# Kernel tuning notes

Hardware: AMD Instinct MI355X
Metric: run time of the kernel (lower is better)

Reference implementation:

```python
import jax, jax.numpy as jnp
import numpy as np

INPUT_SIZE = 64
HIDDEN_SIZE = 512
OUTPUT_SIZE = 1
BATCH = 128
SEQ = 1024


def setup_inputs() -> dict:
    key = jax.random.key(0)
    ks = jax.random.split(key, 7)
    H, I, O = HIDDEN_SIZE, INPUT_SIZE, OUTPUT_SIZE
    s = 1.0 / np.sqrt(H)  # PyTorch LSTM init scale
    x = jax.random.normal(ks[0], (BATCH, SEQ, I), dtype=jnp.float32)
    W_ih = jax.random.uniform(ks[1], (4 * H, I), minval=-s, maxval=s, dtype=jnp.float32)
    W_hh = jax.random.uniform(ks[2], (4 * H, H), minval=-s, maxval=s, dtype=jnp.float32)
    b_ih = jax.random.uniform(ks[3], (4 * H,), minval=-s, maxval=s, dtype=jnp.float32)
    b_hh = jax.random.uniform(ks[4], (4 * H,), minval=-s, maxval=s, dtype=jnp.float32)
    W_fc = jax.random.uniform(ks[5], (O, H), minval=-s, maxval=s, dtype=jnp.float32)
    b_fc = jax.random.uniform(ks[6], (O,), minval=-s, maxval=s, dtype=jnp.float32)
    return {"x": x, "W_ih": W_ih, "W_hh": W_hh, "b_ih": b_ih, "b_hh": b_hh,
            "W_fc": W_fc, "b_fc": b_fc}


def _lstm(x, W_ih, W_hh, b_ih, b_hh):
    # x: [B, T, I]; gate order in PyTorch is (i, f, g, o) along the 4H axis.
    B = x.shape[0]
    H = W_hh.shape[1]
    # Precompute input contribution for all timesteps: [B, T, 4H] -> [T, B, 4H]
    xW = jnp.einsum('bti,gi->btg', x, W_ih) + b_ih + b_hh
    xW = jnp.swapaxes(xW, 0, 1)

    def step(carry, xt):
        h, c = carry
        gates = xt + h @ W_hh.T  # [B, 4H]
        i, f, g, o = jnp.split(gates, 4, axis=-1)
        i = jax.nn.sigmoid(i)
        f = jax.nn.sigmoid(f)
        g = jnp.tanh(g)
        o = jax.nn.sigmoid(o)
        c = f * c + i * g
        h = o * jnp.tanh(c)
        return (h, c), h

    h0 = jnp.zeros((B, H), dtype=x.dtype)
    c0 = jnp.zeros((B, H), dtype=x.dtype)
    _, h_seq = jax.lax.scan(step, (h0, c0), xW)  # [T, B, H]
    return jnp.swapaxes(h_seq, 0, 1)  # [B, T, H]


def reference(x, W_ih, W_hh, b_ih, b_hh, W_fc, b_fc):
    h = _lstm(x, W_ih, W_hh, b_ih, b_hh)          # [B, T, H]
    return jnp.einsum('bth,oh->bto', h, W_fc) + b_fc  # [B, T, O]
```

## Files before the change

### kernel.cpp

```cpp
#include <hip/hip_runtime.h>
#include <hip/hip_cooperative_groups.h>

namespace cg = cooperative_groups;

#define BB 128
#define TT 1024
#define II 64
#define HH 512
#define KK 576
#define NBLK 256
#define NTHR 256

__global__ __launch_bounds__(NTHR, 1)
void lstm_persist(const float* __restrict__ x,
                  const float* __restrict__ W_ih,
                  const float* __restrict__ W_hh,
                  const float* __restrict__ b_ih,
                  const float* __restrict__ b_hh,
                  const float* __restrict__ W_fc,
                  const float* __restrict__ b_fc,
                  float* __restrict__ out,
                  float* __restrict__ hbuf )
{
    __shared__ float Wl[8][KK];
    __shared__ float vx[BB][68];
    __shared__ float gl[8][BB];
    __shared__ float cl[2][BB];
    __shared__ float yl[2][BB];
    __shared__ float wfc[HH];
    __shared__ float bias[8];

    const int u  = threadIdx.x;
    const int g  = blockIdx.x;
    const int j0 = g << 1;

    for (int r = 0; r < 8; ++r) {
        const int R = (r >> 1) * HH + j0 + (r & 1);
        for (int k = u; k < KK; k += NTHR)
            Wl[r][k] = (k < II) ? W_ih[(size_t)R * II + k]
                                : W_hh[(size_t)R * HH + (k - II)];
    }
    if (u < 8) {
        const int R = (u >> 1) * HH + j0 + (u & 1);
        bias[u] = b_ih[R] + b_hh[R];
    }
    for (int k = u; k < HH; k += NTHR) wfc[k] = W_fc[k];
    if (u < BB) { cl[0][u] = 0.f; cl[1][u] = 0.f; }
    if (u < BB) {
        hbuf[(size_t)u * HH + j0]     = 0.f;
        hbuf[(size_t)u * HH + j0 + 1] = 0.f;
    }

    const float bfc  = b_fc[0];
    const bool  doy  = (g == 0);
    const int   bA   = u & 63, bB = bA + 64;
    const int   rp   = u >> 6;
    const int   rA   = rp << 1, rB = rA + 1;

    cg::this_grid().sync();

    for (int t = 0; t <= TT; ++t) {
        const float* __restrict__ hsrc = hbuf + (size_t)(t & 1) * BB * HH;
        float*       __restrict__ hdst = hbuf + (size_t)((t + 1) & 1) * BB * HH;

        float a00 = 0.f, a01 = 0.f, a10 = 0.f, a11 = 0.f;
        float yacc = 0.f;

        const int ch0 = (t == TT) ? 1 : 0;
        for (int ch = ch0; ch < 9; ++ch) {
            if (ch == 0) {
                #pragma unroll
                for (int r8 = 0; r8 < 8; ++r8) {
                    const int flat = u + NTHR * r8;
                    const int b = flat >> 4, q = flat & 15;
                    const float4 v = *(const float4*)(x + ((size_t)b * TT + t) * II + (q << 2));
                    *(float4*)&vx[b][q << 2] = v;
                }
            } else {
                const int k0 = (ch - 1) << 6;
                #pragma unroll
                for (int r8 = 0; r8 < 8; ++r8) {
                    const int flat = u + NTHR * r8;
                    const int b = flat >> 4, q = flat & 15;
                    const float4 v = *(const float4*)(hsrc + (size_t)b * HH + k0 + (q << 2));
                    *(float4*)&vx[b][q << 2] = v;
                }
            }
            __syncthreads();

            if (t < TT) {
                const float* __restrict__ wra = &Wl[rA][ch << 6];
                const float* __restrict__ wrb = &Wl[rB][ch << 6];
                const float* __restrict__ va  = &vx[bA][0];
                const float* __restrict__ vb  = &vx[bB][0];
                #pragma unroll
                for (int k4 = 0; k4 < 16; ++k4) {
                    const float4 wa = *(const float4*)(wra + (k4 << 2));
                    const float4 wb = *(const float4*)(wrb + (k4 << 2));
                    const float4 pa = *(const float4*)(va + (k4 << 2));
                    const float4 pb = *(const float4*)(vb + (k4 << 2));
                    a00 += wa.x*pa.x + wa.y*pa.y + wa.z*pa.z + wa.w*pa.w;
                    a01 += wa.x*pb.x + wa.y*pb.y + wa.z*pb.z + wa.w*pb.w;
                    a10 += wb.x*pa.x + wb.y*pa.y + wb.z*pa.z + wb.w*pa.w;
                    a11 += wb.x*pb.x + wb.y*pb.y + wb.z*pb.z + wb.w*pb.w;
                }
            }
            if (doy && t > 0 && ch > 0) {
                const int b = u & 127, half = u >> 7;
                const float* __restrict__ wf = &wfc[((ch - 1) << 6) + (half << 5)];
                const float* __restrict__ vv = &vx[b][half << 5];
                #pragma unroll
                for (int k4 = 0; k4 < 8; ++k4) {
                    const float4 f4 = *(const float4*)(wf + (k4 << 2));
                    const float4 v4 = *(const float4*)(vv + (k4 << 2));
                    yacc += f4.x*v4.x + f4.y*v4.y + f4.z*v4.z + f4.w*v4.w;
                }
            }
            __syncthreads();
        }

        if (doy && t > 0) {
            const int b = u & 127, half = u >> 7;
            yl[half][b] = yacc;
        }

        if (t == TT) {
            __syncthreads();
            if (doy && u < BB) out[(size_t)u * TT + (TT - 1)] = yl[0][u] + yl[1][u] + bfc;
            break;
        }

        gl[rA][bA] = a00 + bias[rA];
        gl[rA][bB] = a01 + bias[rA];
        gl[rB][bA] = a10 + bias[rB];
        gl[rB][bB] = a11 + bias[rB];
        __syncthreads();

        {
            const int b = u & 127, jj = u >> 7;
            const float gi = gl[0 + jj][b];
            const float gf = gl[2 + jj][b];
            const float gg = gl[4 + jj][b];
            const float go = gl[6 + jj][b];
            const float si = 1.f / (1.f + expf(-gi));
            const float sf = 1.f / (1.f + expf(-gf));
            const float tg = tanhf(gg);
            const float so = 1.f / (1.f + expf(-go));
            const float c  = sf * cl[jj][b] + si * tg;
            cl[jj][b] = c;
            hdst[(size_t)b * HH + j0 + jj] = so * tanhf(c);
            if (doy && t > 0 && u < BB)
                out[(size_t)u * TT + (t - 1)] = yl[0][u] + yl[1][u] + bfc;
        }

        __threadfence();
        cg::this_grid().sync();
    }
}

extern "C" void kernel_launch(void* const* d_in, const int* in_sizes, int n_in,
                              void* d_out, int out_size, void* d_ws, size_t ws_size,
                              hipStream_t stream) {
    const float* x    = (const float*)d_in[0];
    const float* W_ih = (const float*)d_in[1];
    const float* W_hh = (const float*)d_in[2];
    const float* b_ih = (const float*)d_in[3];
    const float* b_hh = (const float*)d_in[4];
    const float* W_fc = (const float*)d_in[5];
    const float* b_fc = (const float*)d_in[6];
    float* out  = (float*)d_out;
    float* hbuf = (float*)d_ws;

    void* args[] = {(void*)&x, (void*)&W_ih, (void*)&W_hh, (void*)&b_ih,
                    (void*)&b_hh, (void*)&W_fc, (void*)&b_fc, (void*)&out,
                    (void*)&hbuf};
    hipLaunchCooperativeKernel((const void*)lstm_persist, dim3(NBLK), dim3(NTHR),
                               args, 0, stream);
}
```

Measured before the change: 78.99 ms.

## Replace cooperative grid sync with hierarchical atomic barrier and register prefetch

Swaps cg::this_grid().sync() for a custom two-level atomic barrier: eight sub-counters, each reached by 32 blocks, feed a master counter that block leaders poll with s_sleep. The next timestep's x loads are issued between barrier arrive and wait so they overlap the wait. The h chunks are prefetched into registers one chunk ahead of the shared-memory stage, the cell state moves from shared memory into a register, and the final output projection is split out of the loop. In exchange it relies on all blocks being co-resident, falls back to a non-cooperative launch that could deadlock, and adds a memset of the barrier counters on every call.

New measurement: 82.62 ms. +4.6%, slower.

```diff
diff --git a/kernel.cpp b/kernel.cpp
--- a/kernel.cpp
+++ b/kernel.cpp
@@ -1,7 +1,4 @@
 #include <hip/hip_runtime.h>
-#include <hip/hip_cooperative_groups.h>
-
-namespace cg = cooperative_groups;
 
 #define BB 128
 #define TT 1024
@@ -20,12 +17,12 @@
                   const float* __restrict__ W_fc,
                   const float* __restrict__ b_fc,
                   float* __restrict__ out,
-                  float* __restrict__ hbuf )
+                  float* __restrict__ hbuf,
+                  unsigned* __restrict__ bar)
 {
     __shared__ float Wl[8][KK];
     __shared__ float vx[BB][68];
     __shared__ float gl[8][BB];
-    __shared__ float cl[2][BB];
     __shared__ float yl[2][BB];
     __shared__ float wfc[HH];
     __shared__ float bias[8];
@@ -33,6 +30,10 @@
     const int u  = threadIdx.x;
     const int g  = blockIdx.x;
     const int j0 = g << 1;
+
+    unsigned epoch = 0;
+    unsigned* __restrict__ subc   = bar + ((g & 7) << 5);
+    unsigned* __restrict__ master = bar + 256;
 
     for (int r = 0; r < 8; ++r) {
         const int R = (r >> 1) * HH + j0 + (r & 1);
@@ -45,54 +46,73 @@
         bias[u] = b_ih[R] + b_hh[R];
     }
     for (int k = u; k < HH; k += NTHR) wfc[k] = W_fc[k];
-    if (u < BB) { cl[0][u] = 0.f; cl[1][u] = 0.f; }
     if (u < BB) {
         hbuf[(size_t)u * HH + j0]     = 0.f;
         hbuf[(size_t)u * HH + j0 + 1] = 0.f;
     }
 
-    const float bfc  = b_fc[0];
-    const bool  doy  = (g == 0);
-    const int   bA   = u & 63, bB = bA + 64;
-    const int   rp   = u >> 6;
-    const int   rA   = rp << 1, rB = rA + 1;
-
-    cg::this_grid().sync();
-
-    for (int t = 0; t <= TT; ++t) {
+    const float bfc = b_fc[0];
+    const bool  doy = (g == 0);
+    const int   bA  = u & 63, bB2 = bA + 64;
+    const int   rp  = u >> 6;
+    const int   rA  = rp << 1, rB = rA + 1;
+    const int   ub  = u & 127, ujj = u >> 7;
+    float creg = 0.f;
+    float4 rx[8];
+
+#define BAR_ARRIVE() do { __threadfence(); __syncthreads();                        \
+    if (u == 0) {                                                                  \
+        unsigned old = __hip_atomic_fetch_add(subc, 1u, __ATOMIC_ACQ_REL,          \
+                                              __HIP_MEMORY_SCOPE_AGENT);           \
+        if ((old & 31u) == 31u)                                                    \
+            __hip_atomic_fetch_add(master, 1u, __ATOMIC_RELEASE,                   \
+                                   __HIP_MEMORY_SCOPE_AGENT);                      \
+    } ++epoch; } while (0)
+
+#define BAR_WAIT() do {                                                            \
+    if (u == 0) {                                                                  \
+        while (__hip_atomic_load(master, __ATOMIC_RELAXED,                         \
+                                 __HIP_MEMORY_SCOPE_AGENT) < (epoch << 3))         \
+            __builtin_amdgcn_s_sleep(1);                                           \
+    } __syncthreads(); __threadfence(); } while (0)
+
+    BAR_ARRIVE();
+    #pragma unroll
+    for (int r8 = 0; r8 < 8; ++r8) {
+        const int flat = u + NTHR * r8, b = flat >> 4, q = flat & 15;
+        rx[r8] = *(const float4*)(x + ((size_t)b * TT + 0) * II + (q << 2));
+    }
+    BAR_WAIT();
+
+    for (int t = 0; t < TT; ++t) {
         const float* __restrict__ hsrc = hbuf + (size_t)(t & 1) * BB * HH;
         float*       __restrict__ hdst = hbuf + (size_t)((t + 1) & 1) * BB * HH;
 
         float a00 = 0.f, a01 = 0.f, a10 = 0.f, a11 = 0.f;
         float yacc = 0.f;
 
-        const int ch0 = (t == TT) ? 1 : 0;
-        for (int ch = ch0; ch < 9; ++ch) {
-            if (ch == 0) {
+        for (int ch = 0; ch < 9; ++ch) {
+            __syncthreads();
+            #pragma unroll
+            for (int r8 = 0; r8 < 8; ++r8) {
+                const int flat = u + NTHR * r8, b = flat >> 4, q = flat & 15;
+                *(float4*)&vx[b][q << 2] = rx[r8];
+            }
+            if (ch < 8) {
+                const int k0 = ch << 6;
                 #pragma unroll
                 for (int r8 = 0; r8 < 8; ++r8) {
-                    const int flat = u + NTHR * r8;
-                    const int b = flat >> 4, q = flat & 15;
-                    const float4 v = *(const float4*)(x + ((size_t)b * TT + t) * II + (q << 2));
-                    *(float4*)&vx[b][q << 2] = v;
+                    const int flat = u + NTHR * r8, b = flat >> 4, q = flat & 15;
+                    rx[r8] = *(const float4*)(hsrc + (size_t)b * HH + k0 + (q << 2));
                 }
-            } else {
-                const int k0 = (ch - 1) << 6;
-                #pragma unroll
-                for (int r8 = 0; r8 < 8; ++r8) {
-                    const int flat = u + NTHR * r8;
-                    const int b = flat >> 4, q = flat & 15;
-                    const float4 v = *(const float4*)(hsrc + (size_t)b * HH + k0 + (q << 2));
-                    *(float4*)&vx[b][q << 2] = v;
-                }
-            }
-            __syncthreads();
-
-            if (t < TT) {
+            }
+            __syncthreads();
+
+            {
                 const float* __restrict__ wra = &Wl[rA][ch << 6];
                 const float* __restrict__ wrb = &Wl[rB][ch << 6];
                 const float* __restrict__ va  = &vx[bA][0];
-                const float* __restrict__ vb  = &vx[bB][0];
+                const float* __restrict__ vb  = &vx[bB2][0];
                 #pragma unroll
                 for (int k4 = 0; k4 < 16; ++k4) {
                     const float4 wa = *(const float4*)(wra + (k4 << 2));
@@ -106,9 +126,8 @@
                 }
             }
             if (doy && t > 0 && ch > 0) {
-                const int b = u & 127, half = u >> 7;
-                const float* __restrict__ wf = &wfc[((ch - 1) << 6) + (half << 5)];
-                const float* __restrict__ vv = &vx[b][half << 5];
+                const float* __restrict__ wf = &wfc[((ch - 1) << 6) + (ujj << 5)];
+                const float* __restrict__ vv = &vx[ub][ujj << 5];
                 #pragma unroll
                 for (int k4 = 0; k4 < 8; ++k4) {
                     const float4 f4 = *(const float4*)(wf + (k4 << 2));
@@ -116,51 +135,76 @@
                     yacc += f4.x*v4.x + f4.y*v4.y + f4.z*v4.z + f4.w*v4.w;
                 }
             }
-            __syncthreads();
-        }
-
-        if (doy && t > 0) {
-            const int b = u & 127, half = u >> 7;
-            yl[half][b] = yacc;
-        }
-
-        if (t == TT) {
-            __syncthreads();
-            if (doy && u < BB) out[(size_t)u * TT + (TT - 1)] = yl[0][u] + yl[1][u] + bfc;
-            break;
-        }
-
-        gl[rA][bA] = a00 + bias[rA];
-        gl[rA][bB] = a01 + bias[rA];
-        gl[rB][bA] = a10 + bias[rB];
-        gl[rB][bB] = a11 + bias[rB];
+        }
+
+        if (doy && t > 0) yl[ujj][ub] = yacc;
+        gl[rA][bA]  = a00 + bias[rA];
+        gl[rA][bB2] = a01 + bias[rA];
+        gl[rB][bA]  = a10 + bias[rB];
+        gl[rB][bB2] = a11 + bias[rB];
         __syncthreads();
 
         {
-            const int b = u & 127, jj = u >> 7;
-            const float gi = gl[0 + jj][b];
-            const float gf = gl[2 + jj][b];
-            const float gg = gl[4 + jj][b];
-            const float go = gl[6 + jj][b];
+            const float gi = gl[0 + ujj][ub];
+            const float gf = gl[2 + ujj][ub];
+            const float gg = gl[4 + ujj][ub];
+            const float go = gl[6 + ujj][ub];
             const float si = 1.f / (1.f + expf(-gi));
             const float sf = 1.f / (1.f + expf(-gf));
             const float tg = tanhf(gg);
             const float so = 1.f / (1.f + expf(-go));
-            const float c  = sf * cl[jj][b] + si * tg;
-            cl[jj][b] = c;
-            hdst[(size_t)b * HH + j0 + jj] = so * tanhf(c);
+            const float c  = sf * creg + si * tg;
+            creg = c;
+            hdst[(size_t)ub * HH + j0 + ujj] = so * tanhf(c);
             if (doy && t > 0 && u < BB)
                 out[(size_t)u * TT + (t - 1)] = yl[0][u] + yl[1][u] + bfc;
         }
 
-        __threadfence();
-        cg::this_grid().sync();
-    }
+        BAR_ARRIVE();
+        if (t + 1 < TT) {
+            #pragma unroll
+            for (int r8 = 0; r8 < 8; ++r8) {
+                const int flat = u + NTHR * r8, b = flat >> 4, q = flat & 15;
+                rx[r8] = *(const float4*)(x + ((size_t)b * TT + (t + 1)) * II + (q << 2));
+            }
+        }
+        BAR_WAIT();
+    }
+
+    if (doy) {
+        const float* __restrict__ hsrc = hbuf + (size_t)(TT & 1) * BB * HH;
+        float yacc = 0.f;
+        for (int ch = 1; ch < 9; ++ch) {
+            const int k0 = (ch - 1) << 6;
+            __syncthreads();
+            #pragma unroll
+            for (int r8 = 0; r8 < 8; ++r8) {
+                const int flat = u + NTHR * r8, b = flat >> 4, q = flat & 15;
+                *(float4*)&vx[b][q << 2] =
+                    *(const float4*)(hsrc + (size_t)b * HH + k0 + (q << 2));
+            }
+            __syncthreads();
+            const float* __restrict__ wf = &wfc[((ch - 1) << 6) + (ujj << 5)];
+            const float* __restrict__ vv = &vx[ub][ujj << 5];
+            #pragma unroll
+            for (int k4 = 0; k4 < 8; ++k4) {
+                const float4 f4 = *(const float4*)(wf + (k4 << 2));
+                const float4 v4 = *(const float4*)(vv + (k4 << 2));
+                yacc += f4.x*v4.x + f4.y*v4.y + f4.z*v4.z + f4.w*v4.w;
+            }
+        }
+        yl[ujj][ub] = yacc;
+        __syncthreads();
+        if (u < BB) out[(size_t)u * TT + (TT - 1)] = yl[0][u] + yl[1][u] + bfc;
+    }
+#undef BAR_ARRIVE
+#undef BAR_WAIT
 }
 
 extern "C" void kernel_launch(void* const* d_in, const int* in_sizes, int n_in,
                               void* d_out, int out_size, void* d_ws, size_t ws_size,
                               hipStream_t stream) {
+    (void)in_sizes; (void)n_in; (void)out_size; (void)ws_size;
     const float* x    = (const float*)d_in[0];
     const float* W_ih = (const float*)d_in[1];
     const float* W_hh = (const float*)d_in[2];
@@ -168,12 +212,20 @@
     const float* b_hh = (const float*)d_in[4];
     const float* W_fc = (const float*)d_in[5];
     const float* b_fc = (const float*)d_in[6];
-    float* out  = (float*)d_out;
-    float* hbuf = (float*)d_ws;
+    float* out = (float*)d_out;
+
+    unsigned* bar  = (unsigned*)d_ws;
+    float*    hbuf = (float*)((char*)d_ws + 4096);
+
+    hipMemsetAsync(d_ws, 0, 4096, stream);
 
     void* args[] = {(void*)&x, (void*)&W_ih, (void*)&W_hh, (void*)&b_ih,
                     (void*)&b_hh, (void*)&W_fc, (void*)&b_fc, (void*)&out,
-                    (void*)&hbuf};
-    hipLaunchCooperativeKernel((const void*)lstm_persist, dim3(NBLK), dim3(NTHR),
-                               args, 0, stream);
+                    (void*)&hbuf, (void*)&bar};
+    hipError_t e = hipLaunchCooperativeKernel((const void*)lstm_persist,
+                                              dim3(NBLK), dim3(NTHR), args, 0, stream);
+    if (e != hipSuccess) {
+        hipLaunchKernelGGL(lstm_persist, dim3(NBLK), dim3(NTHR), 0, stream,
+                           x, W_ih, W_hh, b_ih, b_hh, W_fc, b_fc, out, hbuf, bar);
+    }
 }
```
